# Performance work log

Measured on AMD Instinct MI355X. Metric: run time of the kernel, lower is better.

Reference implementation:

```python
import jax, jax.numpy as jnp
import numpy as np

BN_EPS = 1e-5


def conv1x1(x, w, b):
    # x: [B,C,H,W] (NCHW), w: [Cout,Cin], b: [Cout]
    return jnp.einsum('bchw,oc->bohw', x, w) + b[None, :, None, None]


def dw_bn(x, w_dw, b_dw, scale, bias, mean, var):
    # depthwise 1x1 conv (per-channel affine) followed by eval-mode BatchNorm
    z = x * w_dw[None, :, None, None] + b_dw[None, :, None, None]
    inv = scale / jnp.sqrt(var + BN_EPS)
    return (z - mean[None, :, None, None]) * inv[None, :, None, None] + bias[None, :, None, None]


def setup_inputs() -> dict:
    B, C, W, H = 16, 728, 38, 38
    key = jax.random.key(0)
    ks = jax.random.split(key, 24)
    s = 1.0 / np.sqrt(C)
    d = {
        'x_FAD': jax.random.normal(ks[0], (B, C, W, H), jnp.float32),
        'x_LFS': jax.random.normal(ks[1], (B, C, W, H), jnp.float32),
        'Wq_fad': jax.random.normal(ks[2], (C, C), jnp.float32) * s,
        'bq_fad': jax.random.normal(ks[3], (C,), jnp.float32) * s,
        'Wq_lfs': jax.random.normal(ks[4], (C, C), jnp.float32) * s,
        'bq_lfs': jax.random.normal(ks[5], (C,), jnp.float32) * s,
        'Wk_fad': jax.random.normal(ks[6], (C, C), jnp.float32) * s,
        'bk_fad': jax.random.normal(ks[7], (C,), jnp.float32) * s,
        'Wk_lfs': jax.random.normal(ks[8], (C, C), jnp.float32) * s,
        'bk_lfs': jax.random.normal(ks[9], (C,), jnp.float32) * s,
        'gamma_fad': jnp.zeros((1,), jnp.float32),
        'gamma_lfs': jnp.zeros((1,), jnp.float32),
        'dw_fad_w': jax.random.normal(ks[10], (C,), jnp.float32),
        'dw_fad_b': jax.random.normal(ks[11], (C,), jnp.float32) * 0.1,
        'dw_lfs_w': jax.random.normal(ks[12], (C,), jnp.float32),
        'dw_lfs_b': jax.random.normal(ks[13], (C,), jnp.float32) * 0.1,
        'fad_bn_scale': jnp.ones((C,), jnp.float32) + 0.1 * jax.random.normal(ks[14], (C,), jnp.float32),
        'fad_bn_bias': 0.1 * jax.random.normal(ks[15], (C,), jnp.float32),
        'fad_bn_mean': 0.1 * jax.random.normal(ks[16], (C,), jnp.float32),
        'fad_bn_var': jnp.abs(jax.random.normal(ks[17], (C,), jnp.float32)) + 0.5,
        'lfs_bn_scale': jnp.ones((C,), jnp.float32) + 0.1 * jax.random.normal(ks[18], (C,), jnp.float32),
        'lfs_bn_bias': 0.1 * jax.random.normal(ks[19], (C,), jnp.float32),
        'lfs_bn_mean': 0.1 * jax.random.normal(ks[20], (C,), jnp.float32),
        'lfs_bn_var': jnp.abs(jax.random.normal(ks[21], (C,), jnp.float32)) + 0.5,
    }
    return d


def reference(x_FAD, x_LFS, Wq_fad, bq_fad, Wq_lfs, bq_lfs, Wk_fad, bk_fad, Wk_lfs, bk_lfs,
              gamma_fad, gamma_lfs, dw_fad_w, dw_fad_b, dw_lfs_w, dw_lfs_b,
              fad_bn_scale, fad_bn_bias, fad_bn_mean, fad_bn_var,
              lfs_bn_scale, lfs_bn_bias, lfs_bn_mean, lfs_bn_var):
    B, C, W, H = x_FAD.shape  # W == H
    q_FAD = conv1x1(x_FAD, Wq_fad, bq_fad).reshape(B * C, W, H)
    q_LFS = conv1x1(x_LFS, Wq_lfs, bq_lfs).reshape(B * C, W, H)
    M_query = jnp.concatenate([q_FAD, q_LFS], axis=2)              # [BC, W, 2H]
    k_FAD = conv1x1(x_FAD, Wk_fad, bk_fad).reshape(B * C, W, H).transpose(0, 2, 1)
    k_LFS = conv1x1(x_LFS, Wk_lfs, bk_lfs).reshape(B * C, W, H).transpose(0, 2, 1)
    M_key = jnp.concatenate([k_FAD, k_LFS], axis=1)                # [BC, 2H, W]
    energy = jnp.einsum('bij,bjk->bik', M_query, M_key)            # [BC, W, W]
    attention = jax.nn.softmax(energy, axis=-1).reshape(B, C, W, W)
    g_lfs = jax.nn.sigmoid(gamma_lfs) * 2.0 - 1.0                  # scalar (shape [1])
    g_fad = jax.nn.sigmoid(gamma_fad) * 2.0 - 1.0
    att_LFS = x_LFS * attention * g_lfs
    y_FAD = x_FAD + dw_bn(att_LFS, dw_fad_w, dw_fad_b, fad_bn_scale, fad_bn_bias, fad_bn_mean, fad_bn_var)
    att_FAD = x_FAD * attention * g_fad
    y_LFS = x_LFS + dw_bn(att_FAD, dw_lfs_w, dw_lfs_b, lfs_bn_scale, lfs_bn_bias, lfs_bn_mean, lfs_bn_var)
    return (y_FAD, y_LFS)
```

## Files before the change

kernel.cpp:

```cpp
#include <hip/hip_runtime.h>

typedef unsigned short u16;
typedef __bf16 bf16x8 __attribute__((ext_vector_type(8)));
typedef u16 u16x8 __attribute__((ext_vector_type(8)));
typedef float floatx4 __attribute__((ext_vector_type(4)));

#define NB 16
#define NC 728
#define HW 38
#define NP 1444
#define NPIX 16819712
#define K2 736
#define P2 1536
#define M2 768

__device__ __forceinline__ u16 f2bf(float f) {
  union { float f; unsigned int i; } v; v.f = f;
  unsigned int r = v.i + 0x7FFFu + ((v.i >> 16) & 1u);
  return (u16)(r >> 16);
}

__device__ __forceinline__ void async16(const u16* g, u16* l) {
  __builtin_amdgcn_global_load_lds((__attribute__((address_space(1))) void*)g,
                                   (__attribute__((address_space(3))) void*)l,
                                   16, 0, 0);
}

__global__ void prep_params(const float* __restrict__ gF, const float* __restrict__ gL,
                            const float* __restrict__ dwfw, const float* __restrict__ dwfb,
                            const float* __restrict__ dwlw, const float* __restrict__ dwlb,
                            const float* __restrict__ fs, const float* __restrict__ fb,
                            const float* __restrict__ fm, const float* __restrict__ fv,
                            const float* __restrict__ ls, const float* __restrict__ lb,
                            const float* __restrict__ lm, const float* __restrict__ lv,
                            float* __restrict__ mulF, float* __restrict__ addF,
                            float* __restrict__ mulL, float* __restrict__ addL) {
  int c = blockIdx.x * 256 + threadIdx.x;
  if (c >= NC) return;
  float gf = 2.f / (1.f + __expf(-gF[0])) - 1.f;
  float gl = 2.f / (1.f + __expf(-gL[0])) - 1.f;
  float invf = fs[c] * rsqrtf(fv[c] + 1e-5f);
  mulF[c] = gl * dwfw[c] * invf;
  addF[c] = (dwfb[c] - fm[c]) * invf + fb[c];
  float invl = ls[c] * rsqrtf(lv[c] + 1e-5f);
  mulL[c] = gf * dwlw[c] * invl;
  addL[c] = (dwlb[c] - lm[c]) * invl + lb[c];
}

__global__ __launch_bounds__(256) void transpose_pad(const float* __restrict__ xF,
                                                     const float* __restrict__ xL,
                                                     u16* __restrict__ xTF,
                                                     u16* __restrict__ xTL,
                                                     int bbase, int ng) {
  __shared__ u16 tile[64][68];
  int z = blockIdx.z;
  int tensor = (z >= ng) ? 1 : 0;
  int bl = z - (tensor ? ng : 0);
  int b = bbase + bl;
  const float* x = tensor ? xL : xF;
  u16* xT = tensor ? xTL : xTF;
  int p0 = blockIdx.x * 64, c0 = blockIdx.y * 64;
  int t = threadIdx.x;
  int pl4 = (t & 15) * 4, csub = t >> 4;
  bool fullp = (p0 + 63) < NP;
#pragma unroll
  for (int it = 0; it < 4; ++it) {
    int cl = it * 16 + csub;
    int c = c0 + cl, p = p0 + pl4;
    u16 o0v = 0, o1 = 0, o2 = 0, o3 = 0;
    if (c < NC) {
      const float* src = &x[(size_t)(b * NC + c) * NP + p];
      if (fullp) {
        float4 v = *(const float4*)src;
        o0v = f2bf(v.x); o1 = f2bf(v.y); o2 = f2bf(v.z); o3 = f2bf(v.w);
      } else {
        if (p + 0 < NP) o0v = f2bf(src[0]);
        if (p + 1 < NP) o1 = f2bf(src[1]);
        if (p + 2 < NP) o2 = f2bf(src[2]);
        if (p + 3 < NP) o3 = f2bf(src[3]);
      }
    }
    tile[cl][pl4] = o0v; tile[cl][pl4 + 1] = o1; tile[cl][pl4 + 2] = o2; tile[cl][pl4 + 3] = o3;
  }
  __syncthreads();
  int cl2 = t & 31, psub = t >> 5;
#pragma unroll
  for (int it = 0; it < 8; ++it) {
    int pl = psub * 8 + it;
    int c = c0 + cl2 * 2;
    if (c < K2) {
      unsigned int v = (unsigned int)tile[cl2 * 2][pl] | (((unsigned int)tile[cl2 * 2 + 1][pl]) << 16);
      *(unsigned int*)&xT[(size_t)(bl * P2 + p0 + pl) * K2 + c] = v;
    }
  }
}

__global__ void pad_weights(const float* __restrict__ W0, const float* __restrict__ W1,
                            const float* __restrict__ W2, const float* __restrict__ W3,
                            u16* __restrict__ Wpad) {
  int combo = blockIdx.y;
  const float* W = combo == 0 ? W0 : combo == 1 ? W1 : combo == 2 ? W2 : W3;
  int idx = blockIdx.x * 256 + threadIdx.x;
  if (idx >= M2 * K2) return;
  int r = idx / K2, c = idx - r * K2;
  u16 v = (r < NC && c < NC) ? f2bf(W[r * NC + c]) : (u16)0;
  Wpad[(size_t)combo * (M2 * K2) + idx] = v;
}

__global__ __launch_bounds__(256) void conv_gemm(const u16* __restrict__ Wpad,
                                                 const u16* __restrict__ xTF,
                                                 const u16* __restrict__ xTL,
                                                 const float* __restrict__ b0, const float* __restrict__ b1,
                                                 const float* __restrict__ b2, const float* __restrict__ b3,
                                                 u16* __restrict__ Qf, u16* __restrict__ Kf,
                                                 u16* __restrict__ Ql, u16* __restrict__ Kl) {
  __shared__ __align__(16) u16 A_lds[128 * 32];
  __shared__ __align__(16) u16 B_lds[128 * 32];
  int t = threadIdx.x;
  int lane = t & 63, w = t >> 6;
  int z = blockIdx.z, bl = z >> 2, combo = z & 3;
  int o0 = blockIdx.y * 128, p0 = blockIdx.x * 128;
  const u16* Wb = Wpad + (size_t)combo * (M2 * K2);
  const u16* Xb = ((combo < 2) ? xTF : xTL) + (size_t)bl * (P2 * K2);
  const float* bias = combo == 0 ? b0 : combo == 1 ? b1 : combo == 2 ? b2 : b3;
  u16* Out = combo == 0 ? Qf : combo == 1 ? Kf : combo == 2 ? Ql : Kl;

  const u16* Ag = Wb + (size_t)(o0 + w * 32 + (lane >> 2)) * K2 + (lane & 3) * 8;
  const u16* Bg = Xb + (size_t)(p0 + w * 32 + (lane >> 2)) * K2 + (lane & 3) * 8;
  u16* Al = A_lds + w * 32 * 32;
  u16* Bl = B_lds + w * 32 * 32;

  floatx4 acc[4][4] = {};
  int wm = w >> 1, wn = w & 1;
  int ln = lane & 15, qd = lane >> 4;
  const u16* Ard = A_lds + (wm * 64 + ln) * 32 + qd * 8;
  const u16* Brd = B_lds + (wn * 64 + ln) * 32 + qd * 8;

  for (int kt = 0; kt < 23; ++kt) {
    int ko = kt * 32;
    async16(Ag + ko, Al);
    async16(Ag + ko + 16 * K2, Al + 16 * 32);
    async16(Bg + ko, Bl);
    async16(Bg + ko + 16 * K2, Bl + 16 * 32);
    __syncthreads();
    bf16x8 af[4], bfv[4];
#pragma unroll
    for (int mt = 0; mt < 4; ++mt) af[mt] = *(const bf16x8*)(Ard + mt * 16 * 32);
#pragma unroll
    for (int nt = 0; nt < 4; ++nt) bfv[nt] = *(const bf16x8*)(Brd + nt * 16 * 32);
#pragma unroll
    for (int mt = 0; mt < 4; ++mt)
#pragma unroll
      for (int nt = 0; nt < 4; ++nt)
        acc[mt][nt] = __builtin_amdgcn_mfma_f32_16x16x32_bf16(af[mt], bfv[nt], acc[mt][nt], 0, 0, 0);
    __syncthreads();
  }

#pragma unroll
  for (int mt = 0; mt < 4; ++mt)
#pragma unroll
    for (int reg = 0; reg < 4; ++reg) {
      int o_r = o0 + wm * 64 + mt * 16 + qd * 4 + reg;
      if (o_r < NC) {
        float bv = bias[o_r];
#pragma unroll
        for (int nt = 0; nt < 4; ++nt) {
          int p_c = p0 + wn * 64 + nt * 16 + ln;
          if (p_c < NP) Out[(size_t)(bl * NC + o_r) * NP + p_c] = f2bf(acc[mt][nt][reg] + bv);
        }
      }
    }
}

__global__ __launch_bounds__(64) void attn_final(const u16* __restrict__ Qf, const u16* __restrict__ Kf,
                                                 const u16* __restrict__ Ql, const u16* __restrict__ Kl,
                                                 const float* __restrict__ xF, const float* __restrict__ xL,
                                                 const float* __restrict__ mulF, const float* __restrict__ addF,
                                                 const float* __restrict__ mulL, const float* __restrict__ addL,
                                                 float* __restrict__ out, int bbase) {
  __shared__ __align__(16) u16 q_lds[48 * 96];
  __shared__ __align__(16) u16 k_lds[48 * 96];
  int bc = blockIdx.x;
  int bl = bc / NC, c = bc - bl * NC;
  int t = threadIdx.x;
  int base = bc * NP;
  int gbase = ((bbase + bl) * NC + c) * NP;

  for (int i = t; i < 38 * 5; i += 64) {
    int r = i / 5, c2 = (i - r * 5) * 2;
    *(unsigned int*)&q_lds[r * 96 + 38 + c2] = 0;
    *(unsigned int*)&q_lds[r * 96 + 86 + c2] = 0;
    *(unsigned int*)&k_lds[r * 96 + 38 + c2] = 0;
    *(unsigned int*)&k_lds[r * 96 + 86 + c2] = 0;
  }

#define STAGE(SRC, DST, COL0)                                              \
  {                                                                        \
    _Pragma("unroll") for (int s = 0; s < 3; ++s) {                        \
      int e0 = (s * 64 + t) * 8;                                           \
      if (e0 < NP) {                                                       \
        u16x8 v = *(const u16x8*)(SRC + base + e0);                        \
        int r = e0 / 38, cc = e0 - r * 38;                                 \
        _Pragma("unroll") for (int j = 0; j < 8; ++j) {                    \
          if (e0 + j < NP) DST[r * 96 + (COL0) + cc] = v[j];               \
          if (++cc == 38) { cc = 0; ++r; }                                 \
        }                                                                  \
      }                                                                    \
    }                                                                      \
  }
  STAGE(Qf, q_lds, 0)
  STAGE(Ql, q_lds, 48)
  STAGE(Kf, k_lds, 0)
  STAGE(Kl, k_lds, 48)
#undef STAGE
  __syncthreads();

  int ln = t & 15, qd = t >> 4;
  floatx4 acc[3][3] = {};
#pragma unroll
  for (int ks = 0; ks < 3; ++ks) {
    bf16x8 af[3], bfv[3];
#pragma unroll
    for (int mt = 0; mt < 3; ++mt) af[mt] = *(const bf16x8*)&q_lds[(mt * 16 + ln) * 96 + ks * 32 + qd * 8];
#pragma unroll
    for (int nt = 0; nt < 3; ++nt) bfv[nt] = *(const bf16x8*)&k_lds[(nt * 16 + ln) * 96 + ks * 32 + qd * 8];
#pragma unroll
    for (int mt = 0; mt < 3; ++mt)
#pragma unroll
      for (int nt = 0; nt < 3; ++nt)
        acc[mt][nt] = __builtin_amdgcn_mfma_f32_16x16x32_bf16(af[mt], bfv[nt], acc[mt][nt], 0, 0, 0);
  }
  float rinv[3][4];
#pragma unroll
  for (int mt = 0; mt < 3; ++mt)
#pragma unroll
    for (int reg = 0; reg < 4; ++reg) {
      float m = -1e30f;
#pragma unroll
      for (int nt = 0; nt < 3; ++nt)
        if (nt * 16 + ln < HW) m = fmaxf(m, acc[mt][nt][reg]);
#pragma unroll
      for (int off = 8; off > 0; off >>= 1) m = fmaxf(m, __shfl_xor(m, off, 16));
      float s = 0.f;
#pragma unroll
      for (int nt = 0; nt < 3; ++nt) {
        float v = (nt * 16 + ln < HW) ? __expf(acc[mt][nt][reg] - m) : 0.f;
        acc[mt][nt][reg] = v;
        s += v;
      }
#pragma unroll
      for (int off = 8; off > 0; off >>= 1) s += __shfl_xor(s, off, 16);
      rinv[mt][reg] = 1.f / s;
    }

  __syncthreads();
  float* att = (float*)q_lds;
#pragma unroll
  for (int mt = 0; mt < 3; ++mt)
#pragma unroll
    for (int reg = 0; reg < 4; ++reg) {
      int i = mt * 16 + qd * 4 + reg;
      if (i < HW) {
#pragma unroll
        for (int nt = 0; nt < 3; ++nt) {
          int k = nt * 16 + ln;
          if (k < HW) att[i * HW + k] = acc[mt][nt][reg] * rinv[mt][reg];
        }
      }
    }
  __syncthreads();

  float mf = mulF[c], adf = addF[c], ml = mulL[c], adl = addL[c];
#pragma unroll
  for (int s = 0; s < 6; ++s) {
    int p = s * 256 + t * 4;
    if (p < NP) {
      float4 a  = *(const float4*)&att[p];
      float4 xf = *(const float4*)&xF[gbase + p];
      float4 xl = *(const float4*)&xL[gbase + p];
      float4 yf, yl;
      yf.x = fmaf(xl.x * a.x, mf, xf.x + adf); yl.x = fmaf(xf.x * a.x, ml, xl.x + adl);
      yf.y = fmaf(xl.y * a.y, mf, xf.y + adf); yl.y = fmaf(xf.y * a.y, ml, xl.y + adl);
      yf.z = fmaf(xl.z * a.z, mf, xf.z + adf); yl.z = fmaf(xf.z * a.z, ml, xl.z + adl);
      yf.w = fmaf(xl.w * a.w, mf, xf.w + adf); yl.w = fmaf(xf.w * a.w, ml, xl.w + adl);
      *(float4*)&out[gbase + p] = yf;
      *(float4*)&out[NPIX + gbase + p] = yl;
    }
  }
}

extern "C" void kernel_launch(void* const* d_in, const int* in_sizes, int n_in,
                              void* d_out, int out_size, void* d_ws, size_t ws_size,
                              hipStream_t stream) {
  (void)in_sizes; (void)n_in; (void)out_size;
  const float* xF   = (const float*)d_in[0];
  const float* xL   = (const float*)d_in[1];
  const float* Wq_f = (const float*)d_in[2];
  const float* bq_f = (const float*)d_in[3];
  const float* Wq_l = (const float*)d_in[4];
  const float* bq_l = (const float*)d_in[5];
  const float* Wk_f = (const float*)d_in[6];
  const float* bk_f = (const float*)d_in[7];
  const float* Wk_l = (const float*)d_in[8];
  const float* bk_l = (const float*)d_in[9];
  const float* gF   = (const float*)d_in[10];
  const float* gL   = (const float*)d_in[11];
  const float* dwfw = (const float*)d_in[12];
  const float* dwfb = (const float*)d_in[13];
  const float* dwlw = (const float*)d_in[14];
  const float* dwlb = (const float*)d_in[15];
  const float* fs   = (const float*)d_in[16];
  const float* fb   = (const float*)d_in[17];
  const float* fm   = (const float*)d_in[18];
  const float* fv   = (const float*)d_in[19];
  const float* ls   = (const float*)d_in[20];
  const float* lb   = (const float*)d_in[21];
  const float* lm   = (const float*)d_in[22];
  const float* lv   = (const float*)d_in[23];

  const size_t small_bytes = 4 * (size_t)NC * sizeof(float);
  const size_t wpad_bytes  = (size_t)4 * M2 * K2 * 2;
  const size_t perb_bytes  = (size_t)2 * P2 * K2 * 2
                           + (size_t)4 * NC * NP * 2;
  int ng = 16;
  while (ng > 4 && small_bytes + wpad_bytes + (size_t)ng * perb_bytes > ws_size) ng >>= 1;

  char* ws = (char*)d_ws;
  size_t off = 0;
  float* mulF = (float*)(ws + off); off += NC * sizeof(float);
  float* addF = (float*)(ws + off); off += NC * sizeof(float);
  float* mulL = (float*)(ws + off); off += NC * sizeof(float);
  float* addL = (float*)(ws + off); off += NC * sizeof(float);
  off = (off + 15) & ~(size_t)15;
  u16* Wpad = (u16*)(ws + off); off += wpad_bytes;
  u16* xTF  = (u16*)(ws + off); off += (size_t)ng * P2 * K2 * 2;
  u16* xTL  = (u16*)(ws + off); off += (size_t)ng * P2 * K2 * 2;
  u16* Qf   = (u16*)(ws + off); off += (size_t)ng * NC * NP * 2;
  u16* Kf   = (u16*)(ws + off); off += (size_t)ng * NC * NP * 2;
  u16* Ql   = (u16*)(ws + off); off += (size_t)ng * NC * NP * 2;
  u16* Kl   = (u16*)(ws + off); off += (size_t)ng * NC * NP * 2;

  prep_params<<<dim3(3), dim3(256), 0, stream>>>(gF, gL, dwfw, dwfb, dwlw, dwlb,
                                                 fs, fb, fm, fv, ls, lb, lm, lv,
                                                 mulF, addF, mulL, addL);
  pad_weights<<<dim3((M2 * K2 + 255) / 256, 4), dim3(256), 0, stream>>>(Wq_f, Wk_f, Wq_l, Wk_l, Wpad);
  for (int g = 0; g < NB; g += ng) {
    transpose_pad<<<dim3(P2 / 64, 12, 2 * ng), dim3(256), 0, stream>>>(xF, xL, xTF, xTL, g, ng);
    conv_gemm<<<dim3(12, 6, 4 * ng), dim3(256), 0, stream>>>(Wpad, xTF, xTL,
                                                             bq_f, bk_f, bq_l, bk_l,
                                                             Qf, Kf, Ql, Kl);
    attn_final<<<dim3(ng * NC), dim3(64), 0, stream>>>(Qf, Kf, Ql, Kl, xF, xL,
                                                       mulF, addF, mulL, addL,
                                                       (float*)d_out, g);
  }
}
```

Measured before the change: 611.5 us.

## Double-buffer conv GEMM LDS tiles and remap workgroups for XCD locality

The conv GEMM now keeps two LDS buffers, so the async global-to-LDS load of the next K tile is issued before the MFMA work on the current tile, and one barrier per iteration is removed. The flat workgroup index is also remapped so consecutive workgroups within each of the 8 XCD groups share the same input tile (Q and K combos from one input side), aiming to improve L2 reuse. This doubles LDS use per block. The ordering relies on the in-loop barrier to make the prefetched data visible before the next iteration reads it.

```diff
diff --git a/kernel.cpp b/kernel.cpp
--- a/kernel.cpp
+++ b/kernel.cpp
@@ -114,35 +114,62 @@
                                                  const float* __restrict__ b2, const float* __restrict__ b3,
                                                  u16* __restrict__ Qf, u16* __restrict__ Kf,
                                                  u16* __restrict__ Ql, u16* __restrict__ Kl) {
-  __shared__ __align__(16) u16 A_lds[128 * 32];
-  __shared__ __align__(16) u16 B_lds[128 * 32];
+  __shared__ __align__(16) u16 A_lds[2][128 * 32];
+  __shared__ __align__(16) u16 B_lds[2][128 * 32];
   int t = threadIdx.x;
   int lane = t & 63, w = t >> 6;
-  int z = blockIdx.z, bl = z >> 2, combo = z & 3;
-  int o0 = blockIdx.y * 128, p0 = blockIdx.x * 128;
+
+  unsigned int f = blockIdx.x + 12u * (blockIdx.y + 12u * blockIdx.z);
+  unsigned int nwg = 144u * gridDim.z;
+  unsigned int q = nwg >> 3;
+  unsigned int wid = (f & 7u) * q + (f >> 3);
+  unsigned int xc = wid % 12u;
+  unsigned int r1 = wid / 12u;
+  unsigned int pt = r1 % 12u;
+  unsigned int zz = r1 / 12u;
+  int bl = (int)(zz >> 1);
+  int th = (int)(zz & 1u);
+  int combo = th * 2 + (xc >= 6u ? 1 : 0);
+  int o0 = (int)(xc % 6u) * 128;
+  int p0 = (int)pt * 128;
+
   const u16* Wb = Wpad + (size_t)combo * (M2 * K2);
-  const u16* Xb = ((combo < 2) ? xTF : xTL) + (size_t)bl * (P2 * K2);
+  const u16* Xb = (th == 0 ? xTF : xTL) + (size_t)bl * (P2 * K2);
   const float* bias = combo == 0 ? b0 : combo == 1 ? b1 : combo == 2 ? b2 : b3;
   u16* Out = combo == 0 ? Qf : combo == 1 ? Kf : combo == 2 ? Ql : Kl;
 
   const u16* Ag = Wb + (size_t)(o0 + w * 32 + (lane >> 2)) * K2 + (lane & 3) * 8;
   const u16* Bg = Xb + (size_t)(p0 + w * 32 + (lane >> 2)) * K2 + (lane & 3) * 8;
-  u16* Al = A_lds + w * 32 * 32;
-  u16* Bl = B_lds + w * 32 * 32;
 
   floatx4 acc[4][4] = {};
   int wm = w >> 1, wn = w & 1;
   int ln = lane & 15, qd = lane >> 4;
-  const u16* Ard = A_lds + (wm * 64 + ln) * 32 + qd * 8;
-  const u16* Brd = B_lds + (wn * 64 + ln) * 32 + qd * 8;
-
+  int rdoff = (wm * 64 + ln) * 32 + qd * 8;
+  int rdoffB = (wn * 64 + ln) * 32 + qd * 8;
+
+  {
+    u16* Al = &A_lds[0][w * 32 * 32];
+    u16* Bl = &B_lds[0][w * 32 * 32];
+    async16(Ag, Al);
+    async16(Ag + 16 * K2, Al + 16 * 32);
+    async16(Bg, Bl);
+    async16(Bg + 16 * K2, Bl + 16 * 32);
+  }
+  __syncthreads();
+
+  int cur = 0;
   for (int kt = 0; kt < 23; ++kt) {
-    int ko = kt * 32;
-    async16(Ag + ko, Al);
-    async16(Ag + ko + 16 * K2, Al + 16 * 32);
-    async16(Bg + ko, Bl);
-    async16(Bg + ko + 16 * K2, Bl + 16 * 32);
-    __syncthreads();
+    if (kt + 1 < 23) {
+      int ko = (kt + 1) * 32;
+      u16* Al = &A_lds[cur ^ 1][w * 32 * 32];
+      u16* Bl = &B_lds[cur ^ 1][w * 32 * 32];
+      async16(Ag + ko, Al);
+      async16(Ag + ko + 16 * K2, Al + 16 * 32);
+      async16(Bg + ko, Bl);
+      async16(Bg + ko + 16 * K2, Bl + 16 * 32);
+    }
+    const u16* Ard = &A_lds[cur][rdoff];
+    const u16* Brd = &B_lds[cur][rdoffB];
     bf16x8 af[4], bfv[4];
 #pragma unroll
     for (int mt = 0; mt < 4; ++mt) af[mt] = *(const bf16x8*)(Ard + mt * 16 * 32);
@@ -154,6 +181,7 @@
       for (int nt = 0; nt < 4; ++nt)
         acc[mt][nt] = __builtin_amdgcn_mfma_f32_16x16x32_bf16(af[mt], bfv[nt], acc[mt][nt], 0, 0, 0);
     __syncthreads();
+    cur ^= 1;
   }
 
 #pragma unroll
@@ -346,9 +374,9 @@
   pad_weights<<<dim3((M2 * K2 + 255) / 256, 4), dim3(256), 0, stream>>>(Wq_f, Wk_f, Wq_l, Wk_l, Wpad);
   for (int g = 0; g < NB; g += ng) {
     transpose_pad<<<dim3(P2 / 64, 12, 2 * ng), dim3(256), 0, stream>>>(xF, xL, xTF, xTL, g, ng);
-    conv_gemm<<<dim3(12, 6, 4 * ng), dim3(256), 0, stream>>>(Wpad, xTF, xTL,
-                                                             bq_f, bk_f, bq_l, bk_l,
-                                                             Qf, Kf, Ql, Kl);
+    conv_gemm<<<dim3(12, 12, 2 * ng), dim3(256), 0, stream>>>(Wpad, xTF, xTL,
+                                                              bq_f, bk_f, bq_l, bk_l,
+                                                              Qf, Kf, Ql, Kl);
     attn_final<<<dim3(ng * NC), dim3(64), 0, stream>>>(Qf, Kf, Ql, Kl, xF, xL,
                                                        mulF, addF, mulL, addL,
                                                        (float*)d_out, g);
```

New measurement: 618.4 us. No clear change (+1.1%).
